# Kernel tuning notes

Hardware: AMD Instinct MI355X
Metric: run time of the kernel (lower is better)

The kernel has to match this reference:

```python
import jax, jax.numpy as jnp
import numpy as np

EMB = 2048
HD = 64            # head_dim
NH = 32            # n_heads
NKV = 8            # n_kv_groups
GS = NH // NKV     # group_size = 4
WIN = 128          # sliding_window
LAYER_IDX = 0      # even -> sliding-window mask active
ROPE_BASE = 10000.0
MAX_SEQ = 4096
YARN_ORIG = 1024.0
YARN_SCALE = 4.0
YARN_BETA_FAST = 32.0
YARN_BETA_SLOW = 1.0


def _rope_tables():
    # YaRN-adjusted RoPE tables, shape [MAX_SEQ, HD]
    freqs = 1.0 / ROPE_BASE ** (np.arange(0, HD, 2, dtype=np.float32) / HD)
    wave_len = 2.0 * np.pi / freqs
    low = YARN_ORIG / YARN_BETA_FAST
    high = YARN_ORIG / YARN_BETA_SLOW
    t = np.clip((wave_len - low) / (high - low), 0.0, 1.0)
    eff = freqs * (1.0 - t) + (freqs / YARN_SCALE) * t
    conc = 0.1 * np.log(YARN_SCALE) + 1.0
    ang = (np.arange(MAX_SEQ, dtype=np.float32)[:, None] * eff[None, :]) * conc
    ang = np.concatenate([ang, ang], axis=-1).astype(np.float32)
    return jnp.sin(ang), jnp.cos(ang)


def _apply_rope(x, sin, cos):
    # x: [B, H, S, D]; sin/cos: [B, S, D] -> broadcast over heads
    sin = sin[:, None, :, :]
    cos = cos[:, None, :, :]
    x1 = x[..., : HD // 2]
    x2 = x[..., HD // 2 :]
    rotated = jnp.concatenate([-x2, x1], axis=-1)
    return x * cos + rotated * sin


def setup_inputs() -> dict:
    key = jax.random.key(0)
    ks = jax.random.split(key, 8)
    B, S = 2, 2048
    s = 0.02
    x = jax.random.normal(ks[0], (B, S, EMB), dtype=jnp.float32)
    Wq = jax.random.normal(ks[1], (NH * HD, EMB), dtype=jnp.float32) * s
    Wk = jax.random.normal(ks[2], (NKV * HD, EMB), dtype=jnp.float32) * s
    Wv = jax.random.normal(ks[3], (NKV * HD, EMB), dtype=jnp.float32) * s
    Wo = jax.random.normal(ks[4], (EMB, NH * HD), dtype=jnp.float32) * s
    bq = jnp.zeros((NH * HD,), dtype=jnp.float32)
    bk = jnp.zeros((NKV * HD,), dtype=jnp.float32)
    bv = jnp.zeros((NKV * HD,), dtype=jnp.float32)
    bo = jnp.zeros((EMB,), dtype=jnp.float32)
    sinks = jax.random.normal(ks[5], (1, NH, 1, 1), dtype=jnp.float32)
    position_ids = jnp.arange(B * S, dtype=jnp.int64 if jax.config.jax_enable_x64 else jnp.int32).reshape(B, S)
    return {"x": x, "Wq": Wq, "bq": bq, "Wk": Wk, "bk": bk, "Wv": Wv, "bv": bv,
            "Wo": Wo, "bo": bo, "sinks": sinks, "position_ids": position_ids}


def reference(x, Wq, bq, Wk, bk, Wv, bv, Wo, bo, sinks, position_ids):
    B, S, _ = x.shape
    sin_t, cos_t = _rope_tables()
    sin = sin_t[position_ids]  # [B, S, HD]
    cos = cos_t[position_ids]

    Q = (x @ Wq.T + bq).reshape(B, S, NH, HD).transpose(0, 2, 1, 3)    # [B,NH,S,D]
    K = (x @ Wk.T + bk).reshape(B, S, NKV, HD).transpose(0, 2, 1, 3)   # [B,NKV,S,D]
    V = (x @ Wv.T + bv).reshape(B, S, NKV, HD).transpose(0, 2, 1, 3)

    Q = _apply_rope(Q, sin, cos)
    K = _apply_rope(K, sin, cos)

    # GQA without materializing repeated K/V: group query heads by kv group
    Qg = Q.reshape(B, NKV, GS, S, HD)
    scores = jnp.einsum('bgqsd,bgtd->bgqst', Qg, K) / np.sqrt(HD).astype(np.float32)

    i = jnp.arange(S)[:, None]
    j = jnp.arange(S)[None, :]
    allowed = (j <= i) & (j > i - WIN)
    scores = jnp.where(allowed, scores, -jnp.inf)

    # attention-sink logit prepended before softmax, then dropped
    sink = jnp.broadcast_to(sinks.reshape(1, NKV, GS, 1, 1), (B, NKV, GS, S, 1))
    full = jnp.concatenate([sink, scores], axis=-1)
    attn = jax.nn.softmax(full, axis=-1)[..., 1:]

    ctx = jnp.einsum('bgqst,bgtd->bgqsd', attn, V)
    ctx = ctx.reshape(B, NH, S, HD).transpose(0, 2, 1, 3).reshape(B, S, NH * HD)
    out = ctx @ Wo.T + bo
    return out
```

## Files before the change

### kernel.cpp

```cpp
#include <hip/hip_runtime.h>

typedef unsigned short u16;
typedef __bf16 bf16x8 __attribute__((ext_vector_type(8)));
typedef float f32x4 __attribute__((ext_vector_type(4)));
typedef unsigned short us8 __attribute__((ext_vector_type(8)));

__device__ inline u16 f2bf(float f) {
    union { float f; unsigned u; } v; v.f = f;
    unsigned r = v.u + 0x7FFFu + ((v.u >> 16) & 1u);
    return (u16)(r >> 16);
}
__device__ inline float bf2f(u16 h) {
    union { unsigned u; float f; } v; v.u = ((unsigned)h) << 16;
    return v.f;
}
__device__ inline f32x4 mfma16(bf16x8 a, bf16x8 b, f32x4 c) {
    return __builtin_amdgcn_mfma_f32_16x16x32_bf16(a, b, c, 0, 0, 0);
}
__device__ inline void gload_lds16(const u16* g, u16* l) {
    __builtin_amdgcn_global_load_lds(
        (const __attribute__((address_space(1))) void*)g,
        (__attribute__((address_space(3))) void*)l, 16, 0, 0);
}
union frag_cast { us8 u; bf16x8 b; };

__global__ __launch_bounds__(256)
void pack_all(const float* __restrict__ x,  const float* __restrict__ Wq,
              const float* __restrict__ Wk, const float* __restrict__ Wv,
              const float* __restrict__ Wo, const float* __restrict__ bq,
              const float* __restrict__ bk, const float* __restrict__ bv,
              u16* __restrict__ xb, u16* __restrict__ Wqkvb,
              u16* __restrict__ Wob, float* __restrict__ bqkv,
              float2* __restrict__ tab)
{
    int blk = blockIdx.x;
    if (blk >= 9217) {
        int idx = (blk - 9217) * 256 + threadIdx.x;
        int d = idx & 31, pos = idx >> 5;
        float ex = (float)d * (1.0f / 32.0f);
        float freq = powf(10000.0f, -ex);
        float wl = 6.2831853071795864f / freq;
        float tt = fminf(fmaxf((wl - 32.0f) * (1.0f / 992.0f), 0.0f), 1.0f);
        float eff = (freq * (1.0f - tt) + 0.25f * freq * tt) * 1.1386294361119891f;
        float ang = (float)pos * eff;
        tab[idx] = make_float2(cosf(ang), sinf(ang));
        return;
    }
    if (blk == 9216) {
        for (int k = threadIdx.x; k < 3072; k += 256) {
            float v;
            if (k < 2048) v = bq[k];
            else if (k < 2560) v = bk[k - 2048];
            else v = bv[k - 2560];
            bqkv[k] = v;
        }
        return;
    }
    const float* src; u16* dst; size_t off;
    if (blk < 4096)      { src = x;  dst = xb;                 off = (size_t)blk * 2048; }
    else if (blk < 6144) { src = Wq; dst = Wqkvb;              off = (size_t)(blk - 4096) * 2048; }
    else if (blk < 6656) { src = Wk; dst = Wqkvb + 4194304;    off = (size_t)(blk - 6144) * 2048; }
    else if (blk < 7168) { src = Wv; dst = Wqkvb + 5242880;    off = (size_t)(blk - 6656) * 2048; }
    else                 { src = Wo; dst = Wob;                off = (size_t)(blk - 7168) * 2048; }
    size_t i = off + (size_t)threadIdx.x * 8;
    float4 v0 = *(const float4*)(src + i);
    float4 v1 = *(const float4*)(src + i + 4);
    us8 w;
    w[0] = f2bf(v0.x); w[1] = f2bf(v0.y); w[2] = f2bf(v0.z); w[3] = f2bf(v0.w);
    w[4] = f2bf(v1.x); w[5] = f2bf(v1.y); w[6] = f2bf(v1.z); w[7] = f2bf(v1.w);
    *(us8*)(dst + i) = w;
}

template<int NF, int OUT_BF16>
__global__ __launch_bounds__(512, 2)
void gemm_256(const u16* __restrict__ A, const u16* __restrict__ B,
              const float* __restrict__ bias, void* __restrict__ Yv,
              int M, int N, int K)
{
    constexpr int BUFU = 8192 + 2048 * NF;
    __shared__ u16 lds[4 * BUFU];

    const int tid = threadIdx.x;
    const int lane = tid & 63;
    const int w = tid >> 6;
    const int wr = w >> 2;
    const int wc = w & 3;
    const long m0 = (long)blockIdx.y * 256;
    const long n0 = (long)blockIdx.x * (64 * NF);
    const int cc = lane & 15, qq = lane >> 4;
    const int csw = (qq ^ ((cc >> 1) & 3)) << 3;

    const int sr = lane >> 2;
    const int colsw = ((lane & 3) ^ ((lane >> 3) & 3)) << 3;
    const u16* gA0 = A + (m0 + w * 16 + sr) * (long)K + colsw;
    const u16* gA1 = gA0 + 128 * (long)K;
    const u16* gB0 = B + (n0 + w * 16 + sr) * (long)K + colsw;
    const u16* gB1 = gB0 + 128 * (long)K;
    const bool b2 = (NF == 3) && (w < 4);

    const int NT = K >> 5;

    auto STAGE = [&](int tt) {
        u16* Ab = &lds[(tt & 3) * BUFU];
        u16* Bb = Ab + 8192;
        const int k0 = tt << 5;
        gload_lds16(gA0 + k0, Ab + w * 512);
        gload_lds16(gA1 + k0, Ab + (8 + w) * 512);
        gload_lds16(gB0 + k0, Bb + w * 512);
        if (b2) gload_lds16(gB1 + k0, Bb + (8 + w) * 512);
    };

    f32x4 acc[8][NF];
#pragma unroll
    for (int i = 0; i < 8; i++)
#pragma unroll
        for (int j = 0; j < NF; j++) acc[i][j] = (f32x4){0.f, 0.f, 0.f, 0.f};

    STAGE(0);
    if (NT > 1) STAGE(1);
    if (NT > 2) STAGE(2);

    for (int t = 0; t < NT; ++t) {
        asm volatile("s_waitcnt lgkmcnt(0)" ::: "memory");
        if (t < NT - 2)       asm volatile("s_waitcnt vmcnt(6)" ::: "memory");
        else if (t == NT - 2) asm volatile("s_waitcnt vmcnt(3)" ::: "memory");
        else                  asm volatile("s_waitcnt vmcnt(0)" ::: "memory");
        __builtin_amdgcn_s_barrier();
        __builtin_amdgcn_sched_barrier(0);

        if (t + 3 < NT) STAGE(t + 3);

        const u16* Ab = &lds[(t & 3) * BUFU];
        const u16* Bb = Ab + 8192;
        bf16x8 afv[8], bfv[NF];
#pragma unroll
        for (int j = 0; j < NF; ++j)
            bfv[j] = *(const bf16x8*)&Bb[(wc * (16 * NF) + j * 16 + cc) * 32 + csw];
#pragma unroll
        for (int i = 0; i < 8; ++i)
            afv[i] = *(const bf16x8*)&Ab[(wr * 128 + i * 16 + cc) * 32 + csw];

        __builtin_amdgcn_s_setprio(1);
#pragma unroll
        for (int i = 0; i < 8; ++i)
#pragma unroll
            for (int j = 0; j < NF; ++j)
                acc[i][j] = mfma16(afv[i], bfv[j], acc[i][j]);
        __builtin_amdgcn_s_setprio(0);
    }

#pragma unroll
    for (int i = 0; i < 8; ++i) {
#pragma unroll
        for (int j = 0; j < NF; ++j) {
            long row = m0 + wr * 128 + i * 16 + qq * 4;
            long col = n0 + wc * (16 * NF) + j * 16 + cc;
            float bvv = bias[col];
#pragma unroll
            for (int r2 = 0; r2 < 4; ++r2) {
                float v = acc[i][j][r2] + bvv;
                if (OUT_BF16)
                    ((u16*)Yv)[(row + r2) * (long)N + col] = f2bf(v);
                else
                    ((float*)Yv)[(row + r2) * (long)N + col] = v;
            }
        }
    }
}

__global__ __launch_bounds__(256)
void v_transpose(const u16* __restrict__ Vt, u16* __restrict__ VbT)
{
    __shared__ u16 tile[64][66];
    int s0 = blockIdx.x * 64;
    int bkv = blockIdx.y;
    int b = bkv >> 3, kv = bkv & 7;
    int t = threadIdx.x;
#pragma unroll
    for (int it = 0; it < 16; ++it) {
        int idx = t + it * 256;
        int s = idx >> 6, d = idx & 63;
        tile[s][d] = Vt[((size_t)(b * 2048 + s0 + s)) * 3072 + 2560 + kv * 64 + d];
    }
    __syncthreads();
#pragma unroll
    for (int it = 0; it < 16; ++it) {
        int idx = t + it * 256;
        int d = idx >> 6, s = idx & 63;
        VbT[((size_t)(bkv * 64 + d)) * 2048 + s0 + s] = tile[s][d];
    }
}

__global__ __launch_bounds__(256, 2)
void attn_win2(const u16* __restrict__ QKVr, const u16* __restrict__ VbT,
               const float2* __restrict__ tab, const int* __restrict__ pid,
               const float* __restrict__ sinks, u16* __restrict__ Ctx)
{
    __shared__ u16 Ks[192 * 72];
    __shared__ u16 Vs[64 * 200];
    __shared__ u16 Pb[4 * 16 * 200];
    const int S = 2048;
    const int tid = threadIdx.x;
    const int lane = tid & 63;
    const int w = tid >> 6;
    const int cc = lane & 15, qq = lane >> 4;
    const int blk = blockIdx.x;
    const int qt = blk & 31;
    const int bkv = blk >> 5;
    const int b = bkv >> 3, kv = bkv & 7;
    const int q0 = qt * 64;
    const int ks0 = q0 - 128;
    const int h = kv * 4 + w;

    {
        const int kcol = 2048 + kv * 64;
#pragma unroll
        for (int it = 0; it < 3; ++it) {
            int c = tid + it * 256;
            int kk = c >> 2, dlo = (c & 3) << 3;
            int sk = ks0 + kk;
            us8 lo = {0, 0, 0, 0, 0, 0, 0, 0};
            us8 hi = {0, 0, 0, 0, 0, 0, 0, 0};
            if (sk >= 0) {
                size_t rowoff = (size_t)(b * S + sk) * 3072 + kcol;
                us8 li = *(const us8*)(QKVr + rowoff + dlo);
                us8 hiQ = *(const us8*)(QKVr + rowoff + dlo + 32);
                int pos = pid[b * S + sk];
                const float2* tp = tab + pos * 32 + dlo;
#pragma unroll
                for (int jj = 0; jj < 8; ++jj) {
                    float2 cs = tp[jj];
                    float x1 = bf2f(li[jj]), x2 = bf2f(hiQ[jj]);
                    lo[jj] = f2bf(x1 * cs.x - x2 * cs.y);
                    hi[jj] = f2bf(x2 * cs.x + x1 * cs.y);
                }
            }
            *(us8*)&Ks[kk * 72 + dlo] = lo;
            *(us8*)&Ks[kk * 72 + dlo + 32] = hi;
        }
    }
    const u16* VtBase = VbT + (size_t)bkv * 64 * S;
#pragma unroll
    for (int it = 0; it < 6; ++it) {
        int c = tid + it * 256;
        int d = c / 24, kc = c % 24;
        int kk0 = kc << 3;
        int sk = ks0 + kk0;
        us8 v = {0, 0, 0, 0, 0, 0, 0, 0};
        if (sk >= 0) v = *(const us8*)(VtBase + (size_t)d * S + sk);
        *(us8*)&Vs[d * 200 + kk0] = v;
    }
    __syncthreads();

    const float sinkv = sinks[h];
    u16* Pw = &Pb[w * 3200];

    for (int i = 0; i < 4; ++i) {
        int m = b * S + q0 + i * 16 + cc;
        const u16* Qrow = QKVr + (size_t)m * 3072 + h * 64;
        us8 qlo = *(const us8*)(Qrow + qq * 8);
        us8 qhi = *(const us8*)(Qrow + 32 + qq * 8);
        int pos = pid[m];
        const float2* tp = tab + pos * 32 + qq * 8;
        frag_cast a0, a1;
#pragma unroll
        for (int jj = 0; jj < 8; ++jj) {
            float2 cs = tp[jj];
            float x1 = bf2f(qlo[jj]), x2 = bf2f(qhi[jj]);
            a0.u[jj] = f2bf(x1 * cs.x - x2 * cs.y);
            a1.u[jj] = f2bf(x2 * cs.x + x1 * cs.y);
        }
        bf16x8 aq0 = a0.b, aq1 = a1.b;

        f32x4 sc[12];
#pragma unroll
        for (int j = 0; j < 12; j++) sc[j] = (f32x4){0.f, 0.f, 0.f, 0.f};
#pragma unroll
        for (int j = 0; j < 12; j++) {
            bf16x8 b0 = *(const bf16x8*)&Ks[(j * 16 + cc) * 72 + qq * 8];
            bf16x8 b1 = *(const bf16x8*)&Ks[(j * 16 + cc) * 72 + 32 + qq * 8];
            sc[j] = mfma16(aq0, b0, sc[j]);
            sc[j] = mfma16(aq1, b1, sc[j]);
        }

#pragma unroll
        for (int r = 0; r < 4; ++r) {
            int qi = i * 16 + qq * 4 + r;
            float sval[12];
            float mx = -3.0e38f;
#pragma unroll
            for (int j = 0; j < 12; j++) {
                int kk = j * 16 + cc;
                float s = sc[j][r] * 0.125f;
                bool ok = (kk > qi) && (kk <= qi + 128) && (ks0 + kk >= 0);
                s = ok ? s : -3.0e38f;
                sval[j] = s;
                mx = fmaxf(mx, s);
            }
#pragma unroll
            for (int off = 1; off < 16; off <<= 1) mx = fmaxf(mx, __shfl_xor(mx, off));
            mx = fmaxf(mx, sinkv);
            float sum = 0.f;
#pragma unroll
            for (int j = 0; j < 12; j++) {
                float p = __expf(sval[j] - mx);
                sval[j] = p;
                sum += p;
            }
#pragma unroll
            for (int off = 1; off < 16; off <<= 1) sum += __shfl_xor(sum, off);
            float rden = 1.0f / (sum + __expf(sinkv - mx));
#pragma unroll
            for (int j = 0; j < 12; j++)
                Pw[(qq * 4 + r) * 200 + j * 16 + cc] = f2bf(sval[j] * rden);
        }

        f32x4 o[4];
#pragma unroll
        for (int jt = 0; jt < 4; jt++) o[jt] = (f32x4){0.f, 0.f, 0.f, 0.f};
#pragma unroll
        for (int ks = 0; ks < 6; ks++) {
            bf16x8 ap = *(const bf16x8*)&Pw[cc * 200 + ks * 32 + qq * 8];
#pragma unroll
            for (int jt = 0; jt < 4; jt++) {
                bf16x8 bv = *(const bf16x8*)&Vs[(jt * 16 + cc) * 200 + ks * 32 + qq * 8];
                o[jt] = mfma16(ap, bv, o[jt]);
            }
        }
#pragma unroll
        for (int jt = 0; jt < 4; jt++) {
#pragma unroll
            for (int r = 0; r < 4; r++) {
                size_t off = ((size_t)(b * S + q0 + i * 16 + qq * 4 + r)) * 2048
                           + h * 64 + jt * 16 + cc;
                Ctx[off] = f2bf(o[jt][r]);
            }
        }
    }
}

extern "C" void kernel_launch(void* const* d_in, const int* in_sizes, int n_in,
                              void* d_out, int out_size, void* d_ws, size_t ws_size,
                              hipStream_t stream)
{
    const float* x    = (const float*)d_in[0];
    const float* Wq   = (const float*)d_in[1];
    const float* bq   = (const float*)d_in[2];
    const float* Wk   = (const float*)d_in[3];
    const float* bk   = (const float*)d_in[4];
    const float* Wv   = (const float*)d_in[5];
    const float* bv   = (const float*)d_in[6];
    const float* Wo   = (const float*)d_in[7];
    const float* bo   = (const float*)d_in[8];
    const float* sinks = (const float*)d_in[9];
    const int*   pid  = (const int*)d_in[10];
    float* out = (float*)d_out;

    char*  ws    = (char*)d_ws;
    u16*   Wqkvb = (u16*)ws;
    u16*   Wob   = (u16*)(ws + 12582912);
    u16*   xb    = (u16*)(ws + 20971520);
    u16*   Ctx   = xb;
    u16*   QKVr  = (u16*)(ws + 37748736);
    u16*   VbT   = (u16*)(ws + 62914560);
    float* bqkv  = (float*)(ws + 67108864);
    float2* tab  = (float2*)(ws + 67121152);

    pack_all<<<9729, 256, 0, stream>>>(x, Wq, Wk, Wv, Wo, bq, bk, bv,
                                       xb, Wqkvb, Wob, bqkv, tab);

    gemm_256<3, 1><<<dim3(16, 16), 512, 0, stream>>>(xb, Wqkvb, bqkv, QKVr,
                                                     4096, 3072, 2048);

    v_transpose<<<dim3(32, 16), 256, 0, stream>>>(QKVr, VbT);

    attn_win2<<<512, 256, 0, stream>>>(QKVr, VbT, tab, pid, sinks, Ctx);

    gemm_256<2, 0><<<dim3(16, 16), 512, 0, stream>>>(Ctx, Wob, bo, out,
                                                     4096, 2048, 2048);
}
```

Baseline: 252.4 us.

## Replace 256-row GEMM tiles with 128x128 tiles and XCD-aware block swizzle

```diff
diff --git a/kernel.cpp b/kernel.cpp
--- a/kernel.cpp
+++ b/kernel.cpp
@@ -71,90 +71,88 @@
     *(us8*)(dst + i) = w;
 }
 
-template<int NF, int OUT_BF16>
-__global__ __launch_bounds__(512, 2)
-void gemm_256(const u16* __restrict__ A, const u16* __restrict__ B,
+template<int NBX, int OUT_BF16>
+__global__ __launch_bounds__(256, 3)
+void gemm_128(const u16* __restrict__ A, const u16* __restrict__ B,
               const float* __restrict__ bias, void* __restrict__ Yv,
               int M, int N, int K)
 {
-    constexpr int BUFU = 8192 + 2048 * NF;
-    __shared__ u16 lds[4 * BUFU];
+    __shared__ u16 lds[3 * 8192];
 
     const int tid = threadIdx.x;
     const int lane = tid & 63;
     const int w = tid >> 6;
-    const int wr = w >> 2;
-    const int wc = w & 3;
-    const long m0 = (long)blockIdx.y * 256;
-    const long n0 = (long)blockIdx.x * (64 * NF);
+    const int wr = w >> 1, wc = w & 1;
+    const int wg = blockIdx.x;
+    const int cpx = (NBX * 32) >> 3;
+    const int swz = (wg & 7) * cpx + (wg >> 3);
+    const int by = swz / NBX, bx = swz - by * NBX;
+    const long m0 = (long)by * 128;
+    const long n0 = (long)bx * 128;
     const int cc = lane & 15, qq = lane >> 4;
     const int csw = (qq ^ ((cc >> 1) & 3)) << 3;
 
     const int sr = lane >> 2;
     const int colsw = ((lane & 3) ^ ((lane >> 3) & 3)) << 3;
     const u16* gA0 = A + (m0 + w * 16 + sr) * (long)K + colsw;
-    const u16* gA1 = gA0 + 128 * (long)K;
+    const u16* gA1 = gA0 + 64 * (long)K;
     const u16* gB0 = B + (n0 + w * 16 + sr) * (long)K + colsw;
-    const u16* gB1 = gB0 + 128 * (long)K;
-    const bool b2 = (NF == 3) && (w < 4);
+    const u16* gB1 = gB0 + 64 * (long)K;
 
     const int NT = K >> 5;
 
-    auto STAGE = [&](int tt) {
-        u16* Ab = &lds[(tt & 3) * BUFU];
-        u16* Bb = Ab + 8192;
-        const int k0 = tt << 5;
-        gload_lds16(gA0 + k0, Ab + w * 512);
-        gload_lds16(gA1 + k0, Ab + (8 + w) * 512);
-        gload_lds16(gB0 + k0, Bb + w * 512);
-        if (b2) gload_lds16(gB1 + k0, Bb + (8 + w) * 512);
+    auto STAGE = [&](int k0, int bi) {
+        u16* buf = &lds[bi * 8192];
+        gload_lds16(gA0 + k0, buf + w * 512);
+        gload_lds16(gA1 + k0, buf + (4 + w) * 512);
+        gload_lds16(gB0 + k0, buf + (8 + w) * 512);
+        gload_lds16(gB1 + k0, buf + (12 + w) * 512);
     };
 
-    f32x4 acc[8][NF];
-#pragma unroll
-    for (int i = 0; i < 8; i++)
-#pragma unroll
-        for (int j = 0; j < NF; j++) acc[i][j] = (f32x4){0.f, 0.f, 0.f, 0.f};
-
-    STAGE(0);
-    if (NT > 1) STAGE(1);
-    if (NT > 2) STAGE(2);
-
+    f32x4 acc[4][4];
+#pragma unroll
+    for (int i = 0; i < 4; i++)
+#pragma unroll
+        for (int j = 0; j < 4; j++) acc[i][j] = (f32x4){0.f, 0.f, 0.f, 0.f};
+
+    STAGE(0, 0);
+    int bR = 0;
     for (int t = 0; t < NT; ++t) {
-        asm volatile("s_waitcnt lgkmcnt(0)" ::: "memory");
-        if (t < NT - 2)       asm volatile("s_waitcnt vmcnt(6)" ::: "memory");
-        else if (t == NT - 2) asm volatile("s_waitcnt vmcnt(3)" ::: "memory");
-        else                  asm volatile("s_waitcnt vmcnt(0)" ::: "memory");
+        int bW = bR + 1; if (bW == 3) bW = 0;
+        if (t + 1 < NT) {
+            STAGE((t + 1) << 5, bW);
+            asm volatile("s_waitcnt vmcnt(4)" ::: "memory");
+        } else {
+            asm volatile("s_waitcnt vmcnt(0)" ::: "memory");
+        }
         __builtin_amdgcn_s_barrier();
         __builtin_amdgcn_sched_barrier(0);
 
-        if (t + 3 < NT) STAGE(t + 3);
-
-        const u16* Ab = &lds[(t & 3) * BUFU];
-        const u16* Bb = Ab + 8192;
-        bf16x8 afv[8], bfv[NF];
-#pragma unroll
-        for (int j = 0; j < NF; ++j)
-            bfv[j] = *(const bf16x8*)&Bb[(wc * (16 * NF) + j * 16 + cc) * 32 + csw];
-#pragma unroll
-        for (int i = 0; i < 8; ++i)
-            afv[i] = *(const bf16x8*)&Ab[(wr * 128 + i * 16 + cc) * 32 + csw];
+        const u16* Ab = &lds[bR * 8192];
+        bf16x8 af[4], bfr[4];
+#pragma unroll
+        for (int j = 0; j < 4; ++j)
+            bfr[j] = *(const bf16x8*)&Ab[4096 + (wc * 64 + j * 16 + cc) * 32 + csw];
+#pragma unroll
+        for (int i = 0; i < 4; ++i)
+            af[i] = *(const bf16x8*)&Ab[(wr * 64 + i * 16 + cc) * 32 + csw];
 
         __builtin_amdgcn_s_setprio(1);
 #pragma unroll
-        for (int i = 0; i < 8; ++i)
-#pragma unroll
-            for (int j = 0; j < NF; ++j)
-                acc[i][j] = mfma16(afv[i], bfv[j], acc[i][j]);
+        for (int i = 0; i < 4; ++i)
+#pragma unroll
+            for (int j = 0; j < 4; ++j)
+                acc[i][j] = mfma16(af[i], bfr[j], acc[i][j]);
         __builtin_amdgcn_s_setprio(0);
-    }
-
-#pragma unroll
-    for (int i = 0; i < 8; ++i) {
-#pragma unroll
-        for (int j = 0; j < NF; ++j) {
-            long row = m0 + wr * 128 + i * 16 + qq * 4;
-            long col = n0 + wc * (16 * NF) + j * 16 + cc;
+        bR = bW;
+    }
+
+#pragma unroll
+    for (int i = 0; i < 4; ++i) {
+#pragma unroll
+        for (int j = 0; j < 4; ++j) {
+            long row = m0 + wr * 64 + i * 16 + qq * 4;
+            long col = n0 + wc * 64 + j * 16 + cc;
             float bvv = bias[col];
 #pragma unroll
             for (int r2 = 0; r2 < 4; ++r2) {
@@ -369,13 +367,13 @@
     pack_all<<<9729, 256, 0, stream>>>(x, Wq, Wk, Wv, Wo, bq, bk, bv,
                                        xb, Wqkvb, Wob, bqkv, tab);
 
-    gemm_256<3, 1><<<dim3(16, 16), 512, 0, stream>>>(xb, Wqkvb, bqkv, QKVr,
-                                                     4096, 3072, 2048);
+    gemm_128<24, 1><<<768, 256, 0, stream>>>(xb, Wqkvb, bqkv, QKVr,
+                                             4096, 3072, 2048);
 
     v_transpose<<<dim3(32, 16), 256, 0, stream>>>(QKVr, VbT);
 
     attn_win2<<<512, 256, 0, stream>>>(QKVr, VbT, tab, pid, sinks, Ctx);
 
-    gemm_256<2, 0><<<dim3(16, 16), 512, 0, stream>>>(Ctx, Wob, bo, out,
-                                                     4096, 2048, 2048);
-}
+    gemm_128<16, 0><<<512, 256, 0, stream>>>(Ctx, Wob, bo, out,
+                                             4096, 2048, 2048);
+}
```

Result: slower. 263.6 us (+4.4%).
